# Performance work log

Hardware: AMD Instinct MI355X
Metric: run time of the kernel (lower is better)

Reference implementation:

```python
import jax, jax.numpy as jnp
import numpy as np

SCALE, Z, X, Y = 4, 9, 9, 9
INV_SQRT_2PI = 1.0 / np.sqrt(2.0 * np.pi)


def setup_inputs() -> dict:
    key = jax.random.key(0)
    k1, = jax.random.split(key, 1)
    inp = jax.random.normal(k1, (1, 1, 128, 512, 512), dtype=jnp.float32)
    return {
        "inp": inp,
        "mu_z": jnp.asarray(0.0, dtype=jnp.float32),
        "sig_z": jnp.asarray(0.1, dtype=jnp.float32),
        "bet_xy": jnp.asarray(2.0, dtype=jnp.float32),
        "bet_z": jnp.asarray(1.5, dtype=jnp.float32),
    }


def _gen_alf(bet_xy, bet_z):
    # squared distances along each axis; torch's loop overwrites the wrap-around
    # write, so the net result for odd sizes is simply (arange - size//2)**2
    zd = ((jnp.arange(Z) - Z // 2) ** 2).astype(jnp.float32)[:, None, None]
    xd = ((jnp.arange(X) - X // 2) ** 2).astype(jnp.float32)[None, :, None]
    yd = ((jnp.arange(Y) - Y // 2) ** 2).astype(jnp.float32)[None, None, :]
    d_2 = zd / bet_z ** 2 + (xd + yd) / bet_xy ** 2  # (Z, X, Y)
    return jnp.exp(-d_2 / 2) * INV_SQRT_2PI


def reference(inp, mu_z, sig_z, bet_xy, bet_z):
    z0 = jnp.exp(mu_z + 0.5 * sig_z ** 2)
    rec = inp * z0  # (N, 1, D, H, W)
    alf = _gen_alf(bet_xy, bet_z)[None, None]  # (1, 1, Z, X, Y)
    pad_z = (Z - SCALE + 1) // 2
    rec = jax.lax.conv_general_dilated(
        rec, alf,
        window_strides=(SCALE, 1, 1),
        padding=[(pad_z, pad_z), (X // 2, X // 2), (Y // 2, Y // 2)],
        dimension_numbers=("NCDHW", "OIDHW", "NCDHW"),
    )  # (N, 1, D//SCALE, H, W)
    rec = (rec - rec.min()) / (rec.max() - rec.min())
    return rec
```

## Files before the change

kernel.cpp:

```cpp
#include <hip/hip_runtime.h>

#define D_IN  128
#define D_OUT 32
#define H     512
#define W     512
#define W4    128
#define HB    16
#define ZR    (HB + 8)
#define NTHR  512
#define CONV_GRID (D_OUT * (H / HB))

__global__ __launch_bounds__(NTHR)
void conv3d_fused(const float* __restrict__ inp, float* __restrict__ out,
                  const float* __restrict__ bxy_p, const float* __restrict__ bz_p,
                  float* __restrict__ blkMin, float* __restrict__ blkMax) {
    __shared__ float zbuf[ZR * W];
    __shared__ float smin[8], smax[8];

    const int d  = blockIdx.x >> 5;
    const int h0 = (blockIdx.x & 31) * HB;

    const float bz = bz_p[0], bx = bxy_p[0];
    const float iz = 1.0f / (2.0f * bz * bz);
    const float ix = 1.0f / (2.0f * bx * bx);
    float wz[9], wx[9];
#pragma unroll
    for (int k = 0; k < 9; ++k) {
        float dd = (float)(k - 4);
        wz[k] = expf(-dd * dd * iz);
        wx[k] = expf(-dd * dd * ix);
    }

    const float4* in4 = (const float4*)inp;
    float4* z4 = (float4*)zbuf;

    const int dinBase = 4 * d - 3;
    const bool interior = (d >= 1) && (d <= 30);

    for (int t = threadIdx.x; t < ZR * W4; t += NTHR) {
        int r  = t >> 7;
        int c4 = t & (W4 - 1);
        int h  = h0 - 4 + r;
        float4 acc = make_float4(0.f, 0.f, 0.f, 0.f);
        if ((unsigned)h < H) {
            const float4* p = in4 + (ptrdiff_t)dinBase * (H * W4) + h * W4 + c4;
            if (interior) {
                float4 vv[9];
#pragma unroll
                for (int k = 0; k < 9; ++k) vv[k] = p[k * (H * W4)];
                __builtin_amdgcn_sched_barrier(0);
#pragma unroll
                for (int k = 0; k < 9; ++k) {
                    acc.x += vv[k].x * wz[k]; acc.y += vv[k].y * wz[k];
                    acc.z += vv[k].z * wz[k]; acc.w += vv[k].w * wz[k];
                }
            } else {
#pragma unroll
                for (int k = 0; k < 9; ++k) {
                    int din = dinBase + k;
                    if ((unsigned)din < D_IN) {
                        float4 v = p[k * (H * W4)];
                        acc.x += v.x * wz[k]; acc.y += v.y * wz[k];
                        acc.z += v.z * wz[k]; acc.w += v.w * wz[k];
                    }
                }
            }
        }
        z4[t] = acc;
    }
    __syncthreads();

    const int lane = threadIdx.x & 63;
    float lmin =  3.402823466e38f;
    float lmax = -3.402823466e38f;
    float4* out4 = (float4*)out;

    for (int t = threadIdx.x; t < HB * W4; t += NTHR) {
        int r  = t >> 7;
        int c4 = t & (W4 - 1);

        float4 v = make_float4(0.f, 0.f, 0.f, 0.f);
#pragma unroll
        for (int k = 0; k < 9; ++k) {
            float4 z = z4[(r + k) * W4 + c4];
            v.x += z.x * wx[k]; v.y += z.y * wx[k];
            v.z += z.z * wx[k]; v.w += z.w * wx[k];
        }

        float4 va, vc;
        va.x = __shfl_up(v.x, 1, 64);  va.y = __shfl_up(v.y, 1, 64);
        va.z = __shfl_up(v.z, 1, 64);  va.w = __shfl_up(v.w, 1, 64);
        vc.x = __shfl_down(v.x, 1, 64); vc.y = __shfl_down(v.y, 1, 64);
        vc.z = __shfl_down(v.z, 1, 64); vc.w = __shfl_down(v.w, 1, 64);

        if (lane == 0 || lane == 63) {
            int c4n = c4 + ((lane == 0) ? -1 : 1);
            float4 vn = make_float4(0.f, 0.f, 0.f, 0.f);
            if ((unsigned)c4n < W4) {
#pragma unroll
                for (int k = 0; k < 9; ++k) {
                    float4 z = z4[(r + k) * W4 + c4n];
                    vn.x += z.x * wx[k]; vn.y += z.y * wx[k];
                    vn.z += z.z * wx[k]; vn.w += z.w * wx[k];
                }
            }
            if (lane == 0) va = vn; else vc = vn;
        }

        float win[12] = {va.x, va.y, va.z, va.w,
                         v.x,  v.y,  v.z,  v.w,
                         vc.x, vc.y, vc.z, vc.w};
        float4 o = make_float4(0.f, 0.f, 0.f, 0.f);
#pragma unroll
        for (int k = 0; k < 9; ++k) {
            o.x += win[k]     * wx[k];
            o.y += win[k + 1] * wx[k];
            o.z += win[k + 2] * wx[k];
            o.w += win[k + 3] * wx[k];
        }
        out4[(d * H + h0 + r) * W4 + c4] = o;
        lmin = fminf(lmin, fminf(fminf(o.x, o.y), fminf(o.z, o.w)));
        lmax = fmaxf(lmax, fmaxf(fmaxf(o.x, o.y), fmaxf(o.z, o.w)));
    }

#pragma unroll
    for (int off = 32; off > 0; off >>= 1) {
        lmin = fminf(lmin, __shfl_down(lmin, off, 64));
        lmax = fmaxf(lmax, __shfl_down(lmax, off, 64));
    }
    int wv = threadIdx.x >> 6;
    if (lane == 0) { smin[wv] = lmin; smax[wv] = lmax; }
    __syncthreads();
    if (threadIdx.x == 0) {
        float mn = smin[0], mx = smax[0];
#pragma unroll
        for (int i = 1; i < 8; ++i) { mn = fminf(mn, smin[i]); mx = fmaxf(mx, smax[i]); }
        blkMin[blockIdx.x] = mn;
        blkMax[blockIdx.x] = mx;
    }
}

#define NORM_NTHR  256
#define NORM_F4_PER_THR 4
#define NORM_GRID  ((D_OUT * H * W4) / (NORM_NTHR * NORM_F4_PER_THR))

__global__ __launch_bounds__(NORM_NTHR)
void norm_kernel(const float* __restrict__ in, float* __restrict__ out,
                 const float* __restrict__ blkMin, const float* __restrict__ blkMax) {
    float lmin =  3.402823466e38f;
    float lmax = -3.402823466e38f;
    for (int i = threadIdx.x; i < CONV_GRID; i += NORM_NTHR) {
        lmin = fminf(lmin, blkMin[i]);
        lmax = fmaxf(lmax, blkMax[i]);
    }
#pragma unroll
    for (int off = 32; off > 0; off >>= 1) {
        lmin = fminf(lmin, __shfl_down(lmin, off, 64));
        lmax = fmaxf(lmax, __shfl_down(lmax, off, 64));
    }
    __shared__ float smin[4], smax[4];
    int lane = threadIdx.x & 63, wv = threadIdx.x >> 6;
    if (lane == 0) { smin[wv] = lmin; smax[wv] = lmax; }
    __syncthreads();
    float mn  = fminf(fminf(smin[0], smin[1]), fminf(smin[2], smin[3]));
    float mx  = fmaxf(fmaxf(smax[0], smax[1]), fmaxf(smax[2], smax[3]));
    float inv = 1.0f / (mx - mn);

    const float4* in4  = (const float4*)in;
    float4*       out4 = (float4*)out;
    int base = blockIdx.x * (NORM_NTHR * NORM_F4_PER_THR) + threadIdx.x;
#pragma unroll
    for (int j = 0; j < NORM_F4_PER_THR; ++j) {
        int idx = base + j * NORM_NTHR;
        float4 v = in4[idx];
        out4[idx] = make_float4((v.x - mn) * inv, (v.y - mn) * inv,
                                (v.z - mn) * inv, (v.w - mn) * inv);
    }
}

extern "C" void kernel_launch(void* const* d_in, const int* in_sizes, int n_in,
                              void* d_out, int out_size, void* d_ws, size_t ws_size,
                              hipStream_t stream) {
    const float* inp    = (const float*)d_in[0];
    const float* bet_xy = (const float*)d_in[3];
    const float* bet_z  = (const float*)d_in[4];
    float* out = (float*)d_out;

    char* ws = (char*)d_ws;
    float* blkMin = (float*)(ws + 4096);
    float* blkMax = (float*)(ws + 16384);
    float* bufA   = (float*)(ws + 65536);

    conv3d_fused<<<CONV_GRID, NTHR, 0, stream>>>(inp, bufA, bet_xy, bet_z, blkMin, blkMax);
    norm_kernel<<<NORM_GRID, NORM_NTHR, 0, stream>>>(bufA, out, blkMin, blkMax);
}
```

Measured before the change: 233.7 us.

## Fuse conv and min-max normalization into one cooperative kernel with grid sync

The separate normalization kernel is replaced by a grid-wide sync inside the conv kernel. Each block keeps its output tile in registers, reduces the global min/max after the sync, and writes normalized values directly. This removes the intermediate buffer write and re-read plus a second launch. Row tile height grows from 16 to 64, which cuts the z-halo recompute overhead. The cost is large dynamic LDS and many registers (one block per CU), a grid barrier, and reliance on all 256 blocks being co-resident.

```diff
diff --git a/kernel.cpp b/kernel.cpp
--- a/kernel.cpp
+++ b/kernel.cpp
@@ -1,24 +1,30 @@
 #include <hip/hip_runtime.h>
+#include <hip/hip_cooperative_groups.h>
+
+namespace cg = cooperative_groups;
 
 #define D_IN  128
 #define D_OUT 32
 #define H     512
 #define W     512
 #define W4    128
-#define HB    16
+#define HB    64
 #define ZR    (HB + 8)
 #define NTHR  512
-#define CONV_GRID (D_OUT * (H / HB))
+#define NHT   (H / HB)
+#define CONV_GRID (D_OUT * NHT)
 
-__global__ __launch_bounds__(NTHR)
-void conv3d_fused(const float* __restrict__ inp, float* __restrict__ out,
-                  const float* __restrict__ bxy_p, const float* __restrict__ bz_p,
-                  float* __restrict__ blkMin, float* __restrict__ blkMax) {
-    __shared__ float zbuf[ZR * W];
+extern __shared__ float zbuf[];
+
+__global__ __launch_bounds__(NTHR, 2)
+void conv3d_all(const float* __restrict__ inp, float* __restrict__ out,
+                const float* __restrict__ bxy_p, const float* __restrict__ bz_p,
+                float* __restrict__ blkMin, float* __restrict__ blkMax) {
     __shared__ float smin[8], smax[8];
 
-    const int d  = blockIdx.x >> 5;
-    const int h0 = (blockIdx.x & 31) * HB;
+    const int tid = threadIdx.x;
+    const int d  = blockIdx.x >> 3;
+    const int h0 = (blockIdx.x & 7) * HB;
 
     const float bz = bz_p[0], bx = bxy_p[0];
     const float iz = 1.0f / (2.0f * bz * bz);
@@ -37,7 +43,7 @@
     const int dinBase = 4 * d - 3;
     const bool interior = (d >= 1) && (d <= 30);
 
-    for (int t = threadIdx.x; t < ZR * W4; t += NTHR) {
+    for (int t = tid; t < ZR * W4; t += NTHR) {
         int r  = t >> 7;
         int c4 = t & (W4 - 1);
         int h  = h0 - 4 + r;
@@ -70,14 +76,16 @@
     }
     __syncthreads();
 
-    const int lane = threadIdx.x & 63;
+    const int lane = tid & 63;
     float lmin =  3.402823466e38f;
     float lmax = -3.402823466e38f;
-    float4* out4 = (float4*)out;
+    float4 oreg[16];
 
-    for (int t = threadIdx.x; t < HB * W4; t += NTHR) {
-        int r  = t >> 7;
-        int c4 = t & (W4 - 1);
+#pragma unroll
+    for (int j = 0; j < 16; ++j) {
+        int pos = j * NTHR + tid;
+        int r   = pos >> 7;
+        int c4  = pos & (W4 - 1);
 
         float4 v = make_float4(0.f, 0.f, 0.f, 0.f);
 #pragma unroll
@@ -88,8 +96,8 @@
         }
 
         float4 va, vc;
-        va.x = __shfl_up(v.x, 1, 64);  va.y = __shfl_up(v.y, 1, 64);
-        va.z = __shfl_up(v.z, 1, 64);  va.w = __shfl_up(v.w, 1, 64);
+        va.x = __shfl_up(v.x, 1, 64);   va.y = __shfl_up(v.y, 1, 64);
+        va.z = __shfl_up(v.z, 1, 64);   va.w = __shfl_up(v.w, 1, 64);
         vc.x = __shfl_down(v.x, 1, 64); vc.y = __shfl_down(v.y, 1, 64);
         vc.z = __shfl_down(v.z, 1, 64); vc.w = __shfl_down(v.w, 1, 64);
 
@@ -118,7 +126,7 @@
             o.z += win[k + 2] * wx[k];
             o.w += win[k + 3] * wx[k];
         }
-        out4[(d * H + h0 + r) * W4 + c4] = o;
+        oreg[j] = o;
         lmin = fminf(lmin, fminf(fminf(o.x, o.y), fminf(o.z, o.w)));
         lmax = fmaxf(lmax, fmaxf(fmaxf(o.x, o.y), fmaxf(o.z, o.w)));
     }
@@ -128,53 +136,43 @@
         lmin = fminf(lmin, __shfl_down(lmin, off, 64));
         lmax = fmaxf(lmax, __shfl_down(lmax, off, 64));
     }
-    int wv = threadIdx.x >> 6;
+    int wv = tid >> 6;
     if (lane == 0) { smin[wv] = lmin; smax[wv] = lmax; }
     __syncthreads();
-    if (threadIdx.x == 0) {
+    if (tid == 0) {
         float mn = smin[0], mx = smax[0];
 #pragma unroll
         for (int i = 1; i < 8; ++i) { mn = fminf(mn, smin[i]); mx = fmaxf(mx, smax[i]); }
         blkMin[blockIdx.x] = mn;
         blkMax[blockIdx.x] = mx;
     }
-}
 
-#define NORM_NTHR  256
-#define NORM_F4_PER_THR 4
-#define NORM_GRID  ((D_OUT * H * W4) / (NORM_NTHR * NORM_F4_PER_THR))
+    cg::this_grid().sync();
 
-__global__ __launch_bounds__(NORM_NTHR)
-void norm_kernel(const float* __restrict__ in, float* __restrict__ out,
-                 const float* __restrict__ blkMin, const float* __restrict__ blkMax) {
-    float lmin =  3.402823466e38f;
-    float lmax = -3.402823466e38f;
-    for (int i = threadIdx.x; i < CONV_GRID; i += NORM_NTHR) {
-        lmin = fminf(lmin, blkMin[i]);
-        lmax = fmaxf(lmax, blkMax[i]);
-    }
+    float gmn = blkMin[tid & (CONV_GRID - 1)];
+    float gmx = blkMax[tid & (CONV_GRID - 1)];
 #pragma unroll
     for (int off = 32; off > 0; off >>= 1) {
-        lmin = fminf(lmin, __shfl_down(lmin, off, 64));
-        lmax = fmaxf(lmax, __shfl_down(lmax, off, 64));
+        gmn = fminf(gmn, __shfl_down(gmn, off, 64));
+        gmx = fmaxf(gmx, __shfl_down(gmx, off, 64));
     }
-    __shared__ float smin[4], smax[4];
-    int lane = threadIdx.x & 63, wv = threadIdx.x >> 6;
-    if (lane == 0) { smin[wv] = lmin; smax[wv] = lmax; }
+    if (lane == 0) { smin[wv] = gmn; smax[wv] = gmx; }
     __syncthreads();
-    float mn  = fminf(fminf(smin[0], smin[1]), fminf(smin[2], smin[3]));
-    float mx  = fmaxf(fmaxf(smax[0], smax[1]), fmaxf(smax[2], smax[3]));
-    float inv = 1.0f / (mx - mn);
+    float mn = smin[0], mx = smax[0];
+#pragma unroll
+    for (int i = 1; i < 8; ++i) { mn = fminf(mn, smin[i]); mx = fmaxf(mx, smax[i]); }
+    const float inv = 1.0f / (mx - mn);
 
-    const float4* in4  = (const float4*)in;
-    float4*       out4 = (float4*)out;
-    int base = blockIdx.x * (NORM_NTHR * NORM_F4_PER_THR) + threadIdx.x;
+    float4* out4 = (float4*)out;
 #pragma unroll
-    for (int j = 0; j < NORM_F4_PER_THR; ++j) {
-        int idx = base + j * NORM_NTHR;
-        float4 v = in4[idx];
-        out4[idx] = make_float4((v.x - mn) * inv, (v.y - mn) * inv,
-                                (v.z - mn) * inv, (v.w - mn) * inv);
+    for (int j = 0; j < 16; ++j) {
+        int pos = j * NTHR + tid;
+        int r   = pos >> 7;
+        int c4  = pos & (W4 - 1);
+        float4 o = oreg[j];
+        out4[(d * H + h0 + r) * W4 + c4] =
+            make_float4((o.x - mn) * inv, (o.y - mn) * inv,
+                        (o.z - mn) * inv, (o.w - mn) * inv);
     }
 }
 
@@ -188,9 +186,11 @@
 
     char* ws = (char*)d_ws;
     float* blkMin = (float*)(ws + 4096);
-    float* blkMax = (float*)(ws + 16384);
-    float* bufA   = (float*)(ws + 65536);
+    float* blkMax = (float*)(ws + 8192);
 
-    conv3d_fused<<<CONV_GRID, NTHR, 0, stream>>>(inp, bufA, bet_xy, bet_z, blkMin, blkMax);
-    norm_kernel<<<NORM_GRID, NORM_NTHR, 0, stream>>>(bufA, out, blkMin, blkMax);
+    void* args[] = { (void*)&inp, (void*)&out, (void*)&bet_xy, (void*)&bet_z,
+                     (void*)&blkMin, (void*)&blkMax };
+    hipLaunchCooperativeKernel((const void*)conv3d_all,
+                               dim3(CONV_GRID), dim3(NTHR),
+                               args, ZR * W * sizeof(float), stream);
 }
```

Result: slower. 285.8 us (+22.3%).

## Split fused 3D conv into separate z-pass and hw-pass kernels

Applied to the files above, without the earlier changes.

Replaces the single fused kernel with a dedicated z-direction pass. Each thread in that pass streams 21 input slices once and accumulates four strided output depths in registers, writing the z-filtered volume to a global scratch buffer. A second kernel then loads that buffer with row halos into shared memory and applies the separable H/W filter plus the per-block min/max reduction, as before. The aim is to cut the redundant input reads caused by the overlapping z windows and the recomputation over h halos. The cost is an extra global write and read of the intermediate volume and one more kernel launch.

```diff
diff --git a/kernel.cpp b/kernel.cpp
--- a/kernel.cpp
+++ b/kernel.cpp
@@ -5,77 +5,115 @@
 #define H     512
 #define W     512
 #define W4    128
-#define HB    16
-#define ZR    (HB + 8)
-#define NTHR  512
-#define CONV_GRID (D_OUT * (H / HB))
-
-__global__ __launch_bounds__(NTHR)
-void conv3d_fused(const float* __restrict__ inp, float* __restrict__ out,
-                  const float* __restrict__ bxy_p, const float* __restrict__ bz_p,
-                  float* __restrict__ blkMin, float* __restrict__ blkMax) {
-    __shared__ float zbuf[ZR * W];
-    __shared__ float smin[8], smax[8];
-
-    const int d  = blockIdx.x >> 5;
-    const int h0 = (blockIdx.x & 31) * HB;
-
-    const float bz = bz_p[0], bx = bxy_p[0];
+#define POS   (H * W4)
+
+
+#define ZP_NTHR 512
+#define ZP_K    2
+#define ZP_POSB (ZP_NTHR * ZP_K)
+#define ZP_PT   (POS / ZP_POSB)
+#define ZP_DCH  8
+#define ZP_GRID (ZP_PT * ZP_DCH)
+
+__global__ __launch_bounds__(ZP_NTHR)
+void zpass(const float* __restrict__ inp, float* __restrict__ zout,
+           const float* __restrict__ bz_p) {
+    const int pt   = blockIdx.x & (ZP_PT - 1);
+    const int c    = blockIdx.x / ZP_PT;
+    const int pos0 = pt * ZP_POSB + threadIdx.x;
+
+    const float bz = bz_p[0];
     const float iz = 1.0f / (2.0f * bz * bz);
-    const float ix = 1.0f / (2.0f * bx * bx);
-    float wz[9], wx[9];
+    float wz[9];
 #pragma unroll
     for (int k = 0; k < 9; ++k) {
         float dd = (float)(k - 4);
         wz[k] = expf(-dd * dd * iz);
+    }
+
+    const float4* in4 = (const float4*)inp;
+    float4* zo4 = (float4*)zout;
+
+    float4 acc[4][2];
+#pragma unroll
+    for (int i = 0; i < 4; ++i)
+#pragma unroll
+        for (int j = 0; j < 2; ++j)
+            acc[i][j] = make_float4(0.f, 0.f, 0.f, 0.f);
+
+    const int z0 = 16 * c - 3;
+#pragma unroll
+    for (int s = 0; s < 21; ++s) {
+        const int z = z0 + s;
+        if ((unsigned)z < D_IN) {
+            const float4* p = in4 + (size_t)z * POS + pos0;
+            float4 v0 = p[0];
+            float4 v1 = p[ZP_NTHR];
+#pragma unroll
+            for (int i = 0; i < 4; ++i) {
+                const int k = s - 4 * i;
+                if (k >= 0 && k <= 8) {
+                    const float w = wz[k];
+                    acc[i][0].x += v0.x * w; acc[i][0].y += v0.y * w;
+                    acc[i][0].z += v0.z * w; acc[i][0].w += v0.w * w;
+                    acc[i][1].x += v1.x * w; acc[i][1].y += v1.y * w;
+                    acc[i][1].z += v1.z * w; acc[i][1].w += v1.w * w;
+                }
+            }
+        }
+    }
+
+#pragma unroll
+    for (int i = 0; i < 4; ++i) {
+        const int d = 4 * c + i;
+        zo4[(size_t)d * POS + pos0]           = acc[i][0];
+        zo4[(size_t)d * POS + pos0 + ZP_NTHR] = acc[i][1];
+    }
+}
+
+#define HB    16
+#define ZR    (HB + 8)
+#define HW_NTHR 512
+#define HW_GRID (D_OUT * (H / HB))
+
+__global__ __launch_bounds__(HW_NTHR)
+void hwpass(const float* __restrict__ zin, float* __restrict__ out,
+            const float* __restrict__ bxy_p,
+            float* __restrict__ blkMin, float* __restrict__ blkMax) {
+    __shared__ float zbuf[ZR * W];
+    __shared__ float smin[8], smax[8];
+
+    const int tid = threadIdx.x;
+    const int d  = blockIdx.x >> 5;
+    const int h0 = (blockIdx.x & 31) * HB;
+
+    const float bx = bxy_p[0];
+    const float ix = 1.0f / (2.0f * bx * bx);
+    float wx[9];
+#pragma unroll
+    for (int k = 0; k < 9; ++k) {
+        float dd = (float)(k - 4);
         wx[k] = expf(-dd * dd * ix);
     }
 
-    const float4* in4 = (const float4*)inp;
+    const float4* zin4 = (const float4*)zin;
     float4* z4 = (float4*)zbuf;
 
-    const int dinBase = 4 * d - 3;
-    const bool interior = (d >= 1) && (d <= 30);
-
-    for (int t = threadIdx.x; t < ZR * W4; t += NTHR) {
+    for (int t = tid; t < ZR * W4; t += HW_NTHR) {
         int r  = t >> 7;
         int c4 = t & (W4 - 1);
         int h  = h0 - 4 + r;
-        float4 acc = make_float4(0.f, 0.f, 0.f, 0.f);
-        if ((unsigned)h < H) {
-            const float4* p = in4 + (ptrdiff_t)dinBase * (H * W4) + h * W4 + c4;
-            if (interior) {
-                float4 vv[9];
-#pragma unroll
-                for (int k = 0; k < 9; ++k) vv[k] = p[k * (H * W4)];
-                __builtin_amdgcn_sched_barrier(0);
-#pragma unroll
-                for (int k = 0; k < 9; ++k) {
-                    acc.x += vv[k].x * wz[k]; acc.y += vv[k].y * wz[k];
-                    acc.z += vv[k].z * wz[k]; acc.w += vv[k].w * wz[k];
-                }
-            } else {
-#pragma unroll
-                for (int k = 0; k < 9; ++k) {
-                    int din = dinBase + k;
-                    if ((unsigned)din < D_IN) {
-                        float4 v = p[k * (H * W4)];
-                        acc.x += v.x * wz[k]; acc.y += v.y * wz[k];
-                        acc.z += v.z * wz[k]; acc.w += v.w * wz[k];
-                    }
-                }
-            }
-        }
-        z4[t] = acc;
+        z4[t] = ((unsigned)h < H) ? zin4[(size_t)d * POS + h * W4 + c4]
+                                  : make_float4(0.f, 0.f, 0.f, 0.f);
     }
     __syncthreads();
 
-    const int lane = threadIdx.x & 63;
+    const int lane = tid & 63;
     float lmin =  3.402823466e38f;
     float lmax = -3.402823466e38f;
     float4* out4 = (float4*)out;
 
-    for (int t = threadIdx.x; t < HB * W4; t += NTHR) {
+    for (int t = tid; t < HB * W4; t += HW_NTHR) {
         int r  = t >> 7;
         int c4 = t & (W4 - 1);
 
@@ -88,8 +126,8 @@
         }
 
         float4 va, vc;
-        va.x = __shfl_up(v.x, 1, 64);  va.y = __shfl_up(v.y, 1, 64);
-        va.z = __shfl_up(v.z, 1, 64);  va.w = __shfl_up(v.w, 1, 64);
+        va.x = __shfl_up(v.x, 1, 64);   va.y = __shfl_up(v.y, 1, 64);
+        va.z = __shfl_up(v.z, 1, 64);   va.w = __shfl_up(v.w, 1, 64);
         vc.x = __shfl_down(v.x, 1, 64); vc.y = __shfl_down(v.y, 1, 64);
         vc.z = __shfl_down(v.z, 1, 64); vc.w = __shfl_down(v.w, 1, 64);
 
@@ -118,7 +156,7 @@
             o.z += win[k + 2] * wx[k];
             o.w += win[k + 3] * wx[k];
         }
-        out4[(d * H + h0 + r) * W4 + c4] = o;
+        out4[((size_t)d * H + h0 + r) * W4 + c4] = o;
         lmin = fminf(lmin, fminf(fminf(o.x, o.y), fminf(o.z, o.w)));
         lmax = fmaxf(lmax, fmaxf(fmaxf(o.x, o.y), fmaxf(o.z, o.w)));
     }
@@ -128,10 +166,10 @@
         lmin = fminf(lmin, __shfl_down(lmin, off, 64));
         lmax = fmaxf(lmax, __shfl_down(lmax, off, 64));
     }
-    int wv = threadIdx.x >> 6;
+    int wv = tid >> 6;
     if (lane == 0) { smin[wv] = lmin; smax[wv] = lmax; }
     __syncthreads();
-    if (threadIdx.x == 0) {
+    if (tid == 0) {
         float mn = smin[0], mx = smax[0];
 #pragma unroll
         for (int i = 1; i < 8; ++i) { mn = fminf(mn, smin[i]); mx = fmaxf(mx, smax[i]); }
@@ -149,7 +187,7 @@
                  const float* __restrict__ blkMin, const float* __restrict__ blkMax) {
     float lmin =  3.402823466e38f;
     float lmax = -3.402823466e38f;
-    for (int i = threadIdx.x; i < CONV_GRID; i += NORM_NTHR) {
+    for (int i = threadIdx.x; i < HW_GRID; i += NORM_NTHR) {
         lmin = fminf(lmin, blkMin[i]);
         lmax = fmaxf(lmax, blkMax[i]);
     }
@@ -188,9 +226,11 @@
 
     char* ws = (char*)d_ws;
     float* blkMin = (float*)(ws + 4096);
-    float* blkMax = (float*)(ws + 16384);
-    float* bufA   = (float*)(ws + 65536);
-
-    conv3d_fused<<<CONV_GRID, NTHR, 0, stream>>>(inp, bufA, bet_xy, bet_z, blkMin, blkMax);
-    norm_kernel<<<NORM_GRID, NORM_NTHR, 0, stream>>>(bufA, out, blkMin, blkMax);
-}
+    float* blkMax = (float*)(ws + 8192);
+    float* zbufG  = (float*)(ws + 65536);
+    float* bufB   = (float*)(ws + 65536 + 33554432);
+
+    zpass<<<ZP_GRID, ZP_NTHR, 0, stream>>>(inp, zbufG, bet_z);
+    hwpass<<<HW_GRID, HW_NTHR, 0, stream>>>(zbufG, bufB, bet_xy, blkMin, blkMax);
+    norm_kernel<<<NORM_GRID, NORM_NTHR, 0, stream>>>(bufB, out, blkMin, blkMax);
+}
```

Measured after the change: 248.5 us. 1.06x slower.

## Compute two output depth slices per block to share overlapping z-window loads

Applied to the files above, without the earlier changes.

Each block now produces two adjacent output depth slices. It loads 13 input z-planes once instead of 9 twice, since the two 9-tap windows overlap by 5 planes, and keeps the second slice's z-reduced rows in registers until the first slice's H/W convolution has finished. This cuts global input reads by roughly a quarter and halves the grid. In exchange, register pressure rises (six float4 accumulators are held per thread), fewer blocks are available to fill the GPU, and an extra shared-memory pass is added.

```diff
diff --git a/kernel.cpp b/kernel.cpp
--- a/kernel.cpp
+++ b/kernel.cpp
@@ -5,10 +5,12 @@
 #define H     512
 #define W     512
 #define W4    128
+#define POS   (H * W4)
 #define HB    16
 #define ZR    (HB + 8)
 #define NTHR  512
-#define CONV_GRID (D_OUT * (H / HB))
+#define NPOS  6
+#define CONV_GRID ((D_OUT / 2) * (H / HB))
 
 __global__ __launch_bounds__(NTHR)
 void conv3d_fused(const float* __restrict__ inp, float* __restrict__ out,
@@ -17,7 +19,9 @@
     __shared__ float zbuf[ZR * W];
     __shared__ float smin[8], smax[8];
 
-    const int d  = blockIdx.x >> 5;
+    const int tid = threadIdx.x;
+    const int dp = blockIdx.x >> 5;
+    const int d  = 2 * dp;
     const int h0 = (blockIdx.x & 31) * HB;
 
     const float bz = bz_p[0], bx = bxy_p[0];
@@ -33,111 +37,143 @@
 
     const float4* in4 = (const float4*)inp;
     float4* z4 = (float4*)zbuf;
-
-    const int dinBase = 4 * d - 3;
-    const bool interior = (d >= 1) && (d <= 30);
-
-    for (int t = threadIdx.x; t < ZR * W4; t += NTHR) {
-        int r  = t >> 7;
-        int c4 = t & (W4 - 1);
-        int h  = h0 - 4 + r;
-        float4 acc = make_float4(0.f, 0.f, 0.f, 0.f);
-        if ((unsigned)h < H) {
-            const float4* p = in4 + (ptrdiff_t)dinBase * (H * W4) + h * W4 + c4;
+    const float4 f4z = make_float4(0.f, 0.f, 0.f, 0.f);
+
+    int  rowOff[NPOS];
+    bool rowOk[NPOS];
+#pragma unroll
+    for (int j = 0; j < NPOS; ++j) {
+        int pos = j * NTHR + tid;
+        int r   = pos >> 7;
+        int c4  = pos & (W4 - 1);
+        int h   = h0 - 4 + r;
+        rowOk[j]  = (unsigned)h < H;
+        rowOff[j] = h * W4 + c4;
+    }
+
+#define FMA4(A, V, Wc) do { (A).x += (V).x * (Wc); (A).y += (V).y * (Wc); \
+                            (A).z += (V).z * (Wc); (A).w += (V).w * (Wc); } while (0)
+
+    const int z0 = 4 * d - 3;
+    const bool interior = (dp >= 1) && (dp <= 14);
+
+    float4 accN[NPOS];
+
+#pragma unroll
+    for (int j = 0; j < NPOS; ++j) {
+        float4 a0 = f4z, a1 = f4z;
+        if (rowOk[j]) {
             if (interior) {
-                float4 vv[9];
-#pragma unroll
-                for (int k = 0; k < 9; ++k) vv[k] = p[k * (H * W4)];
+                const float4* p = in4 + (size_t)z0 * POS + rowOff[j];
+                float4 vv[7];
+#pragma unroll
+                for (int s = 0; s < 7; ++s) vv[s] = p[s * POS];
                 __builtin_amdgcn_sched_barrier(0);
 #pragma unroll
-                for (int k = 0; k < 9; ++k) {
-                    acc.x += vv[k].x * wz[k]; acc.y += vv[k].y * wz[k];
-                    acc.z += vv[k].z * wz[k]; acc.w += vv[k].w * wz[k];
-                }
+                for (int s = 0; s < 7; ++s) FMA4(a0, vv[s], wz[s]);
+#pragma unroll
+                for (int s = 4; s < 7; ++s) FMA4(a1, vv[s], wz[s - 4]);
+                float4 uu[6];
+#pragma unroll
+                for (int s = 0; s < 6; ++s) uu[s] = p[(s + 7) * POS];
+                __builtin_amdgcn_sched_barrier(0);
+#pragma unroll
+                for (int s = 7; s < 9; ++s)  FMA4(a0, uu[s - 7], wz[s]);
+#pragma unroll
+                for (int s = 7; s < 13; ++s) FMA4(a1, uu[s - 7], wz[s - 4]);
             } else {
 #pragma unroll
-                for (int k = 0; k < 9; ++k) {
-                    int din = dinBase + k;
-                    if ((unsigned)din < D_IN) {
-                        float4 v = p[k * (H * W4)];
-                        acc.x += v.x * wz[k]; acc.y += v.y * wz[k];
-                        acc.z += v.z * wz[k]; acc.w += v.w * wz[k];
+                for (int s = 0; s < 13; ++s) {
+                    int z = z0 + s;
+                    if ((unsigned)z < D_IN) {
+                        float4 v = in4[(size_t)z * POS + rowOff[j]];
+                        if (s <= 8) FMA4(a0, v, wz[s]);
+                        if (s >= 4) FMA4(a1, v, wz[s - 4]);
                     }
                 }
             }
         }
-        z4[t] = acc;
-    }
-    __syncthreads();
-
-    const int lane = threadIdx.x & 63;
+        z4[j * NTHR + tid] = a0;
+        accN[j] = a1;
+    }
+
+    const int lane = tid & 63;
     float lmin =  3.402823466e38f;
     float lmax = -3.402823466e38f;
     float4* out4 = (float4*)out;
 
-    for (int t = threadIdx.x; t < HB * W4; t += NTHR) {
-        int r  = t >> 7;
-        int c4 = t & (W4 - 1);
-
-        float4 v = make_float4(0.f, 0.f, 0.f, 0.f);
-#pragma unroll
-        for (int k = 0; k < 9; ++k) {
-            float4 z = z4[(r + k) * W4 + c4];
-            v.x += z.x * wx[k]; v.y += z.y * wx[k];
-            v.z += z.z * wx[k]; v.w += z.w * wx[k];
+    auto hwconv = [&](int dOut) {
+        for (int t = tid; t < HB * W4; t += NTHR) {
+            int r  = t >> 7;
+            int c4 = t & (W4 - 1);
+
+            float4 v = f4z;
+#pragma unroll
+            for (int k = 0; k < 9; ++k) {
+                float4 z = z4[(r + k) * W4 + c4];
+                FMA4(v, z, wx[k]);
+            }
+
+            float4 va, vc;
+            va.x = __shfl_up(v.x, 1, 64);   va.y = __shfl_up(v.y, 1, 64);
+            va.z = __shfl_up(v.z, 1, 64);   va.w = __shfl_up(v.w, 1, 64);
+            vc.x = __shfl_down(v.x, 1, 64); vc.y = __shfl_down(v.y, 1, 64);
+            vc.z = __shfl_down(v.z, 1, 64); vc.w = __shfl_down(v.w, 1, 64);
+
+            if (lane == 0 || lane == 63) {
+                int c4n = c4 + ((lane == 0) ? -1 : 1);
+                float4 vn = f4z;
+                if ((unsigned)c4n < W4) {
+#pragma unroll
+                    for (int k = 0; k < 9; ++k) {
+                        float4 z = z4[(r + k) * W4 + c4n];
+                        FMA4(vn, z, wx[k]);
+                    }
+                }
+                if (lane == 0) va = vn; else vc = vn;
+            }
+
+            float win[12] = {va.x, va.y, va.z, va.w,
+                             v.x,  v.y,  v.z,  v.w,
+                             vc.x, vc.y, vc.z, vc.w};
+            float4 o = f4z;
+#pragma unroll
+            for (int k = 0; k < 9; ++k) {
+                o.x += win[k]     * wx[k];
+                o.y += win[k + 1] * wx[k];
+                o.z += win[k + 2] * wx[k];
+                o.w += win[k + 3] * wx[k];
+            }
+            out4[((size_t)dOut * H + h0 + r) * W4 + c4] = o;
+            lmin = fminf(lmin, fminf(fminf(o.x, o.y), fminf(o.z, o.w)));
+            lmax = fmaxf(lmax, fmaxf(fmaxf(o.x, o.y), fmaxf(o.z, o.w)));
         }
-
-        float4 va, vc;
-        va.x = __shfl_up(v.x, 1, 64);  va.y = __shfl_up(v.y, 1, 64);
-        va.z = __shfl_up(v.z, 1, 64);  va.w = __shfl_up(v.w, 1, 64);
-        vc.x = __shfl_down(v.x, 1, 64); vc.y = __shfl_down(v.y, 1, 64);
-        vc.z = __shfl_down(v.z, 1, 64); vc.w = __shfl_down(v.w, 1, 64);
-
-        if (lane == 0 || lane == 63) {
-            int c4n = c4 + ((lane == 0) ? -1 : 1);
-            float4 vn = make_float4(0.f, 0.f, 0.f, 0.f);
-            if ((unsigned)c4n < W4) {
-#pragma unroll
-                for (int k = 0; k < 9; ++k) {
-                    float4 z = z4[(r + k) * W4 + c4n];
-                    vn.x += z.x * wx[k]; vn.y += z.y * wx[k];
-                    vn.z += z.z * wx[k]; vn.w += z.w * wx[k];
-                }
-            }
-            if (lane == 0) va = vn; else vc = vn;
-        }
-
-        float win[12] = {va.x, va.y, va.z, va.w,
-                         v.x,  v.y,  v.z,  v.w,
-                         vc.x, vc.y, vc.z, vc.w};
-        float4 o = make_float4(0.f, 0.f, 0.f, 0.f);
-#pragma unroll
-        for (int k = 0; k < 9; ++k) {
-            o.x += win[k]     * wx[k];
-            o.y += win[k + 1] * wx[k];
-            o.z += win[k + 2] * wx[k];
-            o.w += win[k + 3] * wx[k];
-        }
-        out4[(d * H + h0 + r) * W4 + c4] = o;
-        lmin = fminf(lmin, fminf(fminf(o.x, o.y), fminf(o.z, o.w)));
-        lmax = fmaxf(lmax, fmaxf(fmaxf(o.x, o.y), fmaxf(o.z, o.w)));
-    }
+    };
+
+    __syncthreads();
+    hwconv(d);
+    __syncthreads();
+#pragma unroll
+    for (int j = 0; j < NPOS; ++j) z4[j * NTHR + tid] = accN[j];
+    __syncthreads();
+    hwconv(d + 1);
 
 #pragma unroll
     for (int off = 32; off > 0; off >>= 1) {
         lmin = fminf(lmin, __shfl_down(lmin, off, 64));
         lmax = fmaxf(lmax, __shfl_down(lmax, off, 64));
     }
-    int wv = threadIdx.x >> 6;
+    int wv = tid >> 6;
     if (lane == 0) { smin[wv] = lmin; smax[wv] = lmax; }
     __syncthreads();
-    if (threadIdx.x == 0) {
+    if (tid == 0) {
         float mn = smin[0], mx = smax[0];
 #pragma unroll
         for (int i = 1; i < 8; ++i) { mn = fminf(mn, smin[i]); mx = fmaxf(mx, smax[i]); }
         blkMin[blockIdx.x] = mn;
         blkMax[blockIdx.x] = mx;
     }
+#undef FMA4
 }
 
 #define NORM_NTHR  256
@@ -188,7 +224,7 @@
 
     char* ws = (char*)d_ws;
     float* blkMin = (float*)(ws + 4096);
-    float* blkMax = (float*)(ws + 16384);
+    float* blkMax = (float*)(ws + 8192);
     float* bufA   = (float*)(ws + 65536);
 
     conv3d_fused<<<CONV_GRID, NTHR, 0, stream>>>(inp, bufA, bet_xy, bet_z, blkMin, blkMax);
```

Result: slower. 240.1 us (+2.7%).
